# Kernel tuning notes

Hardware: AMD Instinct MI355X
Metric: run time of the kernel (lower is better)

Reference implementation:

```python
import jax, jax.numpy as jnp
import numpy as np

B, S, D, H = 2, 2048, 1024, 16
HD = D // H                      # 64
NUM_ROPE_DIMS = 2
NF = HD // (2 * NUM_ROPE_DIMS)   # 16 freqs per rope dim -> total HD//2
FFN_H = 4 * D


def householder_matrix(vs):
    """Product of Householder reflections: Q = prod_i (I - 2 v_i v_i^T / ||v_i||^2)."""
    dim = vs.shape[-1]
    def step(Q, v):
        v = v[:, None]
        Q = Q - (2.0 / (jnp.sum(v * v) + 1e-8)) * (v @ (v.T @ Q))
        return Q, None
    Q, _ = jax.lax.scan(step, jnp.eye(dim, dtype=vs.dtype), vs)
    return Q


def rmsnorm(x):
    # torch.nn.RMSNorm(eps=None) uses dtype eps, no affine
    return x * jax.lax.rsqrt(jnp.mean(x * x, axis=-1, keepdims=True) + jnp.finfo(x.dtype).eps)


def setup_inputs() -> dict:
    key = jax.random.key(0)
    ks = jax.random.split(key, 8)
    x = jax.random.normal(ks[0], (B, S, D), jnp.float32)
    mask = jnp.tril(jnp.ones((S, S), dtype=bool))          # causal block mask
    qkv_w = jax.random.normal(ks[1], (3 * D, D), jnp.float32) * 0.02
    out_w = jax.random.normal(ks[2], (D, D), jnp.float32) * 0.02
    gate_w = jax.random.normal(ks[3], (D, D), jnp.float32) * 0.02
    gate_b = jnp.zeros((D,), jnp.float32)
    w12 = jax.random.normal(ks[4], (2 * FFN_H, D), jnp.float32) * 0.02
    w3 = jax.random.normal(ks[5], (D, FFN_H), jnp.float32) * 0.02
    hh_vs = jax.random.normal(ks[6], (HD // 2, HD), jnp.float32) * 0.02
    inv_freq = 1.0 / (10000.0 ** (jnp.arange(NF, dtype=jnp.float32) / NF))
    pos = jnp.arange(S, dtype=jnp.float32)
    rope_pos = jnp.stack([pos, pos], axis=-1)              # [S, num_rope_dims]
    return dict(x=x, mask=mask, qkv_w=qkv_w, out_w=out_w, gate_w=gate_w,
                gate_b=gate_b, w12=w12, w3=w3, hh_vs=hh_vs,
                inv_freq=inv_freq, rope_pos=rope_pos)


def reference(x, mask, qkv_w, out_w, gate_w, gate_b, w12, w3, hh_vs, inv_freq, rope_pos):
    Bs, Ss, Ds = x.shape
    resid = x
    xn = rmsnorm(x)
    qkv = xn @ qkv_w.T                                      # [B,S,3D]
    q, k, v = jnp.split(qkv, 3, axis=-1)
    q = q.reshape(Bs, Ss, H, HD).transpose(0, 2, 1, 3)      # [B,H,S,HD]
    k = k.reshape(Bs, Ss, H, HD).transpose(0, 2, 1, 3)
    v = v.reshape(Bs, Ss, H, HD).transpose(0, 2, 1, 3)

    # RnRoPE: rotate into canonical basis, apply RoPE, rotate back
    Q = householder_matrix(hh_vs)                           # [HD,HD]
    q = q @ Q.T
    k = k @ Q.T
    # geo_state.scale = 1.0
    full = jnp.einsum('sd,f->sdf', rope_pos, inv_freq).reshape(Ss, -1)  # [S, HD//2]
    half = HD // 2
    full = full[:, :half]
    emb = jnp.concatenate([full, full], axis=-1)            # [S, HD]
    cos, sin = jnp.cos(emb), jnp.sin(emb)

    def rot(t):
        t1, t2 = jnp.split(t, 2, axis=-1)
        return t * cos + jnp.concatenate([-t2, t1], axis=-1) * sin

    q = rot(q) @ Q
    k = rot(k) @ Q

    # block-masked attention (flex_attention default scale = 1/sqrt(HD))
    scores = jnp.einsum('bhsd,bhtd->bhst', q, k) / jnp.sqrt(jnp.asarray(HD, x.dtype))
    scores = jnp.where(mask, scores, -jnp.inf)
    attn = jax.nn.softmax(scores, axis=-1)
    o = jnp.einsum('bhst,bhtd->bhsd', attn, v)
    o = o.transpose(0, 2, 1, 3).reshape(Bs, Ss, Ds)
    o = o @ out_w.T
    gate = jax.nn.sigmoid(o @ gate_w.T + gate_b)
    x = resid + o * gate

    # SwiGLU FFN
    resid2 = x
    xn2 = rmsnorm(x)
    x12 = xn2 @ w12.T
    x1, x2 = jnp.split(x12, 2, axis=-1)
    ffn = (jax.nn.silu(x1) * x2) @ w3.T
    return resid2 + ffn
```

## Files before the change

kernel.cpp:

```cpp
#include <hip/hip_runtime.h>
#include <hip/hip_bf16.h>
#include <math.h>

constexpr int Bc = 2, Sc = 2048, Dc = 1024, Hc = 16, HDc = 64;
constexpr int D3 = 3 * Dc;

typedef __bf16 bf16x8 __attribute__((ext_vector_type(8)));
typedef float f32x4 __attribute__((ext_vector_type(4)));

__device__ __forceinline__ void gll16(const void* g, void* l) {
  __builtin_amdgcn_global_load_lds((const __attribute__((address_space(1))) unsigned int*)g,
                                   (__attribute__((address_space(3))) unsigned int*)l,
                                   16, 0, 0);
}

__device__ __forceinline__ unsigned short f2bf(float v) {
  __hip_bfloat16 h = __float2bfloat16(v);
  return *(unsigned short*)&h;
}
__device__ __forceinline__ float b2f(unsigned short u) {
  unsigned v = ((unsigned)u) << 16;
  return __uint_as_float(v);
}

#define SBAR() asm volatile("s_barrier" ::: "memory")

__global__ __launch_bounds__(256) void f2b_kernel(const float* __restrict__ in,
                                                  unsigned short* __restrict__ out) {
  int i = blockIdx.x * 256 + threadIdx.x;
  float4 v = ((const float4*)in)[i];
  ushort4 o;
  o.x = f2bf(v.x); o.y = f2bf(v.y); o.z = f2bf(v.z); o.w = f2bf(v.w);
  ((ushort4*)out)[i] = o;
}

__global__ __launch_bounds__(256) void w12i_kernel(const float* __restrict__ in,
                                                   unsigned short* __restrict__ out) {
  int r = blockIdx.x;
  int g = r >> 5, u = r & 31;
  int src = ((u < 16) ? 0 : 4096) + g * 16 + (u & 15);
  float4 v = ((const float4*)(in + (size_t)src * 1024))[threadIdx.x];
  ushort4 o;
  o.x = f2bf(v.x); o.y = f2bf(v.y); o.z = f2bf(v.z); o.w = f2bf(v.w);
  ((ushort4*)(out + (size_t)r * 1024))[threadIdx.x] = o;
}

__global__ __launch_bounds__(256) void rmsnorm_bf16_kernel(const float* __restrict__ in,
                                                           unsigned short* __restrict__ out) {
  int row = blockIdx.x;
  const float4* x4 = (const float4*)(in + (size_t)row * Dc);
  float4 v = x4[threadIdx.x];
  float s = v.x * v.x + v.y * v.y + v.z * v.z + v.w * v.w;
#pragma unroll
  for (int off = 1; off < 64; off <<= 1) s += __shfl_xor(s, off);
  __shared__ float wsum[4];
  if ((threadIdx.x & 63) == 0) wsum[threadIdx.x >> 6] = s;
  __syncthreads();
  float tot = wsum[0] + wsum[1] + wsum[2] + wsum[3];
  float r = rsqrtf(tot * (1.0f / Dc) + 1.1920928955078125e-07f);
  ushort4 o;
  o.x = f2bf(v.x * r); o.y = f2bf(v.y * r); o.z = f2bf(v.z * r); o.w = f2bf(v.w * r);
  ((ushort4*)(out + (size_t)row * Dc))[threadIdx.x] = o;
}

__global__ __launch_bounds__(64) void hh_kernel(const float* __restrict__ vs,
                                                float* __restrict__ Qout) {
  __shared__ float Qm[64][65];
  __shared__ float vsh[64];
  int t = threadIdx.x;
  for (int i = 0; i < 64; ++i) Qm[i][t] = (i == t) ? 1.0f : 0.0f;
  for (int it = 0; it < 32; ++it) {
    __syncthreads();
    vsh[t] = vs[it * 64 + t];
    __syncthreads();
    float nv = 0.0f;
    for (int i = 0; i < 64; ++i) nv += vsh[i] * vsh[i];
    float c = 2.0f / (nv + 1e-8f);
    float wj = 0.0f;
    for (int i = 0; i < 64; ++i) wj += vsh[i] * Qm[i][t];
    for (int i = 0; i < 64; ++i) Qm[i][t] -= c * vsh[i] * wj;
  }
  __syncthreads();
  for (int i = 0; i < 64; ++i) Qout[i * 64 + t] = Qm[i][t];
}

__global__ __launch_bounds__(256) void wqk_kernel(const float* __restrict__ W,
                                                  const float* __restrict__ Qm,
                                                  unsigned short* __restrict__ out) {
  int n = blockIdx.x;
  int r = n & 63;
  int base = n & ~63;
  int t = threadIdx.x;
  float a0 = 0, a1 = 0, a2 = 0, a3 = 0;
  const float4* Wp = (const float4*)(W + (size_t)base * 1024) + t;
#pragma unroll 8
  for (int e = 0; e < 64; ++e) {
    float q = Qm[r * 64 + e];
    float4 wv = Wp[(size_t)e * 256];
    a0 += q * wv.x; a1 += q * wv.y; a2 += q * wv.z; a3 += q * wv.w;
  }
  float sc = (n < 1024) ? 0.18033688f : 1.0f;
  ushort4 o;
  o.x = f2bf(a0 * sc); o.y = f2bf(a1 * sc); o.z = f2bf(a2 * sc); o.w = f2bf(a3 * sc);
  ((ushort4*)(out + (size_t)n * 1024))[t] = o;
}

__global__ __launch_bounds__(256) void rtab_kernel(const float* __restrict__ rope_pos,
                                                   const float* __restrict__ inv_freq,
                                                   float2* __restrict__ tab) {
  int id = blockIdx.x * 256 + threadIdx.x;
  int s = id >> 5, d = id & 31;
  float pos = rope_pos[s * 2 + (d >> 4)];
  float emb = pos * inv_freq[d & 15];
  tab[id] = make_float2(cosf(emb), sinf(emb));
}

__global__ __launch_bounds__(256) void rope_kernel(const unsigned short* __restrict__ qkv,
                                                   const float2* __restrict__ tab,
                                                   unsigned short* __restrict__ qb,
                                                   unsigned short* __restrict__ kb) {
  int t = threadIdx.x;
  int gid = blockIdx.x * 64 + (t >> 2);
  int sub = t & 3;
  int h = gid & 15;
  int which = (gid >> 4) & 1;
  int tok = gid >> 5;
  int s = tok & (Sc - 1), b = tok >> 11;
  const unsigned short* src = qkv + (size_t)tok * D3 + which * Dc + h * 64 + sub * 8;
  uint4 lov = *(const uint4*)src;
  uint4 hiv = *(const uint4*)(src + 32);
  const unsigned short* lp = (const unsigned short*)&lov;
  const unsigned short* hp = (const unsigned short*)&hiv;
  unsigned short olo[8], ohi[8];
  const float2* tp = tab + s * 32 + sub * 8;
#pragma unroll
  for (int i = 0; i < 8; ++i) {
    float2 cs = tp[i];
    float lo = b2f(lp[i]), hi = b2f(hp[i]);
    olo[i] = f2bf(lo * cs.x - hi * cs.y);
    ohi[i] = f2bf(hi * cs.x + lo * cs.y);
  }
  unsigned short* dst = (which ? kb : qb) + ((size_t)((b * Hc + h) * Sc + s)) * 64 + sub * 8;
  *(uint4*)dst = *(uint4*)olo;
  *(uint4*)(dst + 32) = *(uint4*)ohi;
}

__global__ __launch_bounds__(256) void vt_kernel(const unsigned short* __restrict__ qkv,
                                                 unsigned short* __restrict__ vtb) {
  __shared__ unsigned short tile[64 * 72];
  int st = blockIdx.x;
  int bh = blockIdx.y;
  int b = bh >> 4, h = bh & 15;
  int t = threadIdx.x;
  int srow = t >> 2, c16 = (t & 3) * 16;
  const unsigned short* src =
      qkv + (size_t)(b * Sc + st * 64 + srow) * D3 + 2 * Dc + h * 64 + c16;
  uint4 a0 = *(const uint4*)src;
  uint4 a1 = *(const uint4*)(src + 8);
  *(uint4*)(tile + srow * 72 + c16) = a0;
  *(uint4*)(tile + srow * 72 + c16 + 8) = a1;
  __syncthreads();
  int d = t >> 2, sch = (t & 3) * 16;
  unsigned short tmp[16];
#pragma unroll
  for (int i = 0; i < 16; ++i) tmp[i] = tile[(sch + i) * 72 + d];
  unsigned short* dst = vtb + ((size_t)(bh * 64 + d)) * Sc + st * 64 + sch;
  *(uint4*)dst = *(uint4*)tmp;
  *(uint4*)(dst + 8) = *(uint4*)(tmp + 8);
}

template <int MODE>
__global__ __launch_bounds__(512, 1) void mgemm8p(const unsigned short* __restrict__ A,
                                                  const unsigned short* __restrict__ B,
                                                  unsigned short* __restrict__ C,
                                                  int M, int N, int K) {
  __shared__ unsigned short lds[65536];
  const int t = threadIdx.x;
  const int lane = t & 63;
  const int wave = t >> 6;
  const int wr = wave >> 2, wc = wave & 3;
  const int l15 = lane & 15, l4 = lane >> 4;
  const int gx = gridDim.x;
  const int nwg = gx * gridDim.y;
  const int id = blockIdx.y * gx + blockIdx.x;
  const int swz = (id & 7) * (nwg >> 3) + (id >> 3);
  const int m0 = (swz / gx) * 256;
  const int n0 = (swz % gx) * 256;
  const int NT = K >> 6;
  const int sko = (((t & 3) ^ ((t >> 3) & 3)) * 8);
  const unsigned short* ag0 = A + (size_t)(m0 + (t >> 2)) * K + sko;
  const unsigned short* ag1 = ag0 + (size_t)128 * K;
  const unsigned short* bg0 = B + (size_t)(n0 + (t >> 2)) * K + sko;
  const unsigned short* bg1 = bg0 + (size_t)128 * K;
  const int t8 = t * 8;
  const int ks = (l4 ^ ((l15 >> 1) & 3)) * 8;
  gll16(ag0, lds + t8);
  gll16(ag1, lds + 4096 + t8);
  gll16(bg0, lds + 32768 + t8);
  gll16(bg1, lds + 32768 + 4096 + t8);
  gll16(ag0 + 32, lds + 8192 + t8);
  gll16(ag1 + 32, lds + 8192 + 4096 + t8);
  gll16(bg0 + 32, lds + 32768 + 8192 + t8);
  gll16(bg1 + 32, lds + 32768 + 8192 + 4096 + t8);
  asm volatile("s_waitcnt vmcnt(4)" ::: "memory");
  SBAR();
  f32x4 acc[8][4] = {};
  for (int kt = 0; kt < NT; ++kt) {
    const int cur = (kt & 1) << 14;
    const int nxt = cur ^ 16384;
    const int kof = ((kt + 1 < NT) ? (kt + 1) : kt) << 6;
    const unsigned short* Ap = lds + cur;
    const unsigned short* Bp = lds + 32768 + cur;
    bf16x8 a[8], b0, b1;
#pragma unroll
    for (int i = 0; i < 8; ++i)
      a[i] = *(const bf16x8*)(Ap + (wr * 128 + i * 16 + l15) * 32 + ks);
    b0 = *(const bf16x8*)(Bp + (wc * 64 + l15) * 32 + ks);
    b1 = *(const bf16x8*)(Bp + (wc * 64 + 16 + l15) * 32 + ks);
    gll16(ag0 + kof, lds + nxt + t8);
    gll16(ag1 + kof, lds + nxt + 4096 + t8);
    SBAR();
    __builtin_amdgcn_s_setprio(1);
#pragma unroll
    for (int i = 0; i < 8; ++i) {
      acc[i][0] = __builtin_amdgcn_mfma_f32_16x16x32_bf16(a[i], b0, acc[i][0], 0, 0, 0);
      acc[i][1] = __builtin_amdgcn_mfma_f32_16x16x32_bf16(a[i], b1, acc[i][1], 0, 0, 0);
    }
    __builtin_amdgcn_s_setprio(0);
    SBAR();
    b0 = *(const bf16x8*)(Bp + (wc * 64 + 32 + l15) * 32 + ks);
    b1 = *(const bf16x8*)(Bp + (wc * 64 + 48 + l15) * 32 + ks);
    gll16(bg0 + kof, lds + 32768 + nxt + t8);
    gll16(bg1 + kof, lds + 32768 + nxt + 4096 + t8);
    asm volatile("s_waitcnt vmcnt(4)" ::: "memory");
    SBAR();
    __builtin_amdgcn_s_setprio(1);
#pragma unroll
    for (int i = 0; i < 8; ++i) {
      acc[i][2] = __builtin_amdgcn_mfma_f32_16x16x32_bf16(a[i], b0, acc[i][2], 0, 0, 0);
      acc[i][3] = __builtin_amdgcn_mfma_f32_16x16x32_bf16(a[i], b1, acc[i][3], 0, 0, 0);
    }
    __builtin_amdgcn_s_setprio(0);
    SBAR();
#pragma unroll
    for (int i = 0; i < 8; ++i)
      a[i] = *(const bf16x8*)(Ap + 8192 + (wr * 128 + i * 16 + l15) * 32 + ks);
    b0 = *(const bf16x8*)(Bp + 8192 + (wc * 64 + l15) * 32 + ks);
    b1 = *(const bf16x8*)(Bp + 8192 + (wc * 64 + 16 + l15) * 32 + ks);
    gll16(ag0 + kof + 32, lds + nxt + 8192 + t8);
    gll16(ag1 + kof + 32, lds + nxt + 8192 + 4096 + t8);
    SBAR();
    __builtin_amdgcn_s_setprio(1);
#pragma unroll
    for (int i = 0; i < 8; ++i) {
      acc[i][0] = __builtin_amdgcn_mfma_f32_16x16x32_bf16(a[i], b0, acc[i][0], 0, 0, 0);
      acc[i][1] = __builtin_amdgcn_mfma_f32_16x16x32_bf16(a[i], b1, acc[i][1], 0, 0, 0);
    }
    __builtin_amdgcn_s_setprio(0);
    SBAR();
    b0 = *(const bf16x8*)(Bp + 8192 + (wc * 64 + 32 + l15) * 32 + ks);
    b1 = *(const bf16x8*)(Bp + 8192 + (wc * 64 + 48 + l15) * 32 + ks);
    gll16(bg0 + kof + 32, lds + 32768 + nxt + 8192 + t8);
    gll16(bg1 + kof + 32, lds + 32768 + nxt + 8192 + 4096 + t8);
    asm volatile("s_waitcnt vmcnt(4)" ::: "memory");
    SBAR();
    __builtin_amdgcn_s_setprio(1);
#pragma unroll
    for (int i = 0; i < 8; ++i) {
      acc[i][2] = __builtin_amdgcn_mfma_f32_16x16x32_bf16(a[i], b0, acc[i][2], 0, 0, 0);
      acc[i][3] = __builtin_amdgcn_mfma_f32_16x16x32_bf16(a[i], b1, acc[i][3], 0, 0, 0);
    }
    __builtin_amdgcn_s_setprio(0);
    SBAR();
  }
  asm volatile("s_waitcnt vmcnt(0)" ::: "memory");
  const int r0 = m0 + wr * 128 + l4 * 4;
  if (MODE == 0) {
    const int c0 = n0 + wc * 64 + l15;
#pragma unroll
    for (int i = 0; i < 8; ++i)
#pragma unroll
      for (int j = 0; j < 4; ++j)
#pragma unroll
        for (int r = 0; r < 4; ++r)
          C[(size_t)(r0 + i * 16 + r) * N + c0 + j * 16] = f2bf(acc[i][j][r]);
  } else {
    const int nc = N >> 1;
    const int c0 = (n0 >> 1) + wc * 32 + l15;
#pragma unroll
    for (int i = 0; i < 8; ++i)
#pragma unroll
      for (int p = 0; p < 2; ++p)
#pragma unroll
        for (int r = 0; r < 4; ++r) {
          float v = acc[i][2 * p][r];
          float sv = v / (1.0f + __expf(-v));
          C[(size_t)(r0 + i * 16 + r) * nc + c0 + p * 16] = f2bf(sv * acc[i][2 * p + 1][r]);
        }
  }
}

template <int MODE>
__global__ __launch_bounds__(256, 3) void mgemm64(const unsigned short* __restrict__ A,
                                                  const unsigned short* __restrict__ W,
                                                  const float* __restrict__ R,
                                                  const float* __restrict__ R2,
                                                  const float* __restrict__ bias,
                                                  void* __restrict__ Cout,
                                                  void* __restrict__ Cout2,
                                                  int M, int N, int K) {
  __shared__ unsigned short As[2][2048];
  __shared__ unsigned short Bs[2][4096];
  const int t = threadIdx.x;
  const int lane = t & 63;
  const int wave = t >> 6;
  const int wr = wave >> 1, wc = wave & 1;
  const int m0 = blockIdx.y * 64, n0 = blockIdx.x * 128;
  f32x4 acc[2][4] = {};
  const int srow = t >> 2;
  const int sch = (((t & 3) ^ ((t >> 3) & 3)) * 8);
  const unsigned short* Ag = A + (size_t)(m0 + srow) * K + sch;
  const unsigned short* Wg = W + (size_t)(n0 + srow) * K + sch;
  const size_t rstep = (size_t)64 * K;
  const int frow = lane & 15;
  const int l4 = lane >> 4;
  const int fk = (l4 ^ ((frow >> 1) & 3)) * 8;
  gll16(Ag, As[0] + t * 8);
  gll16(Wg, Bs[0] + t * 8);
  gll16(Wg + rstep, Bs[0] + 2048 + t * 8);
  for (int k0 = 0; k0 < K; k0 += 32) {
    const int cur = (k0 >> 5) & 1;
    const int kn = (k0 + 32 < K) ? (k0 + 32) : k0;
    gll16(Ag + kn, As[cur ^ 1] + t * 8);
    gll16(Wg + kn, Bs[cur ^ 1] + t * 8);
    gll16(Wg + kn + rstep, Bs[cur ^ 1] + 2048 + t * 8);
    asm volatile("s_waitcnt vmcnt(3)" ::: "memory");
    SBAR();
    bf16x8 af[2], bq[4];
#pragma unroll
    for (int i = 0; i < 2; ++i)
      af[i] = *(const bf16x8*)(As[cur] + (wr * 32 + i * 16 + frow) * 32 + fk);
#pragma unroll
    for (int j = 0; j < 4; ++j)
      bq[j] = *(const bf16x8*)(Bs[cur] + (wc * 64 + j * 16 + frow) * 32 + fk);
    __builtin_amdgcn_s_setprio(1);
#pragma unroll
    for (int i = 0; i < 2; ++i)
#pragma unroll
      for (int j = 0; j < 4; ++j)
        acc[i][j] = __builtin_amdgcn_mfma_f32_16x16x32_bf16(af[i], bq[j], acc[i][j], 0, 0, 0);
    __builtin_amdgcn_s_setprio(0);
    SBAR();
  }
  asm volatile("s_waitcnt vmcnt(0)" ::: "memory");
  const int crow = wr * 32 + (lane >> 4) * 4;
  const int ccol = wc * 64 + (lane & 15);
#pragma unroll
  for (int i = 0; i < 2; ++i) {
#pragma unroll
    for (int j = 0; j < 4; ++j) {
#pragma unroll
      for (int r = 0; r < 4; ++r) {
        int row = m0 + crow + i * 16 + r;
        int col = n0 + ccol + j * 16;
        float v = acc[i][j][r];
        size_t off = (size_t)row * N + col;
        if (MODE == 2) {
          ((float*)Cout)[off] = v + R[off];
        } else if (MODE == 4) {
          ((float*)Cout)[off] = v;
          ((unsigned short*)Cout2)[off] = f2bf(v);
        } else {
          float g = v + bias[col];
          float sg = 1.0f / (1.0f + __expf(-g));
          ((float*)Cout)[off] = R[off] + R2[off] * sg;
        }
      }
    }
  }
}

__global__ __launch_bounds__(256, 3) void mattn(const unsigned short* __restrict__ qb,
                                                const unsigned short* __restrict__ kb,
                                                const unsigned short* __restrict__ vtb,
                                                unsigned short* __restrict__ out) {
  __shared__ unsigned short Qs[8192];
  __shared__ unsigned short Ks[2][4096];
  __shared__ unsigned short Vts[4096];
  __shared__ unsigned short Ps[4 * 16 * 72];
  const int qt = gridDim.x - 1 - blockIdx.x;
  const int bh = blockIdx.y;
  const int b = bh >> 4, h = bh & 15;
  const int t = threadIdx.x, lane = t & 63, w = t >> 6;
  const int l15 = lane & 15, l4 = lane >> 4;
  const unsigned short* qbase = qb + ((size_t)bh * Sc + qt * 128) * 64;
  const unsigned short* kbase = kb + (size_t)bh * Sc * 64;
  const unsigned short* vbase = vtb + (size_t)bh * 64 * Sc;
#pragma unroll
  for (int i = 0; i < 4; ++i) {
    int idx = t + i * 256;
    int r = idx >> 3;
    int cg = (idx & 7) ^ (r & 7);
    gll16(qbase + (size_t)r * 64 + cg * 8, Qs + idx * 8);
  }
  const int sr = t >> 3;
  const int scg = (t & 7) ^ (sr & 7);
  gll16(vbase + (size_t)sr * Sc + scg * 8, Vts + t * 8);
  gll16(vbase + (size_t)(sr + 32) * Sc + scg * 8, Vts + 2048 + t * 8);
  gll16(kbase + (size_t)sr * 64 + scg * 8, Ks[0] + t * 8);
  gll16(kbase + (size_t)(sr + 32) * 64 + scg * 8, Ks[0] + 2048 + t * 8);
  bf16x8 qf[2][2];
  f32x4 oacc[2][4] = {};
  float lrow[2][4] = {};
  unsigned short* pw = Ps + w * 16 * 72;
  const int ktmax = 2 * qt + 1;
  for (int kt = 0; kt <= ktmax; ++kt) {
    const int cur = kt & 1;
    if (kt > 0) {
      gll16(vbase + (size_t)sr * Sc + kt * 64 + scg * 8, Vts + t * 8);
      gll16(vbase + (size_t)(sr + 32) * Sc + kt * 64 + scg * 8, Vts + 2048 + t * 8);
    }
    const int ktn = (kt < ktmax) ? kt + 1 : kt;
    gll16(kbase + (size_t)(ktn * 64 + sr) * 64 + scg * 8, Ks[cur ^ 1] + t * 8);
    gll16(kbase + (size_t)(ktn * 64 + sr + 32) * 64 + scg * 8, Ks[cur ^ 1] + 2048 + t * 8);
    if (kt == 0) {
      asm volatile("s_waitcnt vmcnt(2)" ::: "memory");
    } else {
      asm volatile("s_waitcnt vmcnt(4)" ::: "memory");
    }
    SBAR();
    if (kt == 0) {
#pragma unroll
      for (int ch = 0; ch < 2; ++ch) {
        int qrow = ch * 64 + w * 16 + l15;
#pragma unroll
        for (int kc = 0; kc < 2; ++kc)
          qf[ch][kc] = *(const bf16x8*)(Qs + qrow * 64 + (((kc * 4 + l4) ^ (l15 & 7)) * 8));
      }
    }
    const bool actA = (kt <= 2 * qt);
    f32x4 sc[2][4] = {};
#pragma unroll
    for (int kc = 0; kc < 2; ++kc) {
      bf16x8 kf[4];
#pragma unroll
      for (int j = 0; j < 4; ++j)
        kf[j] = *(const bf16x8*)(Ks[cur] + (j * 16 + l15) * 64 + (((kc * 4 + l4) ^ (l15 & 7)) * 8));
      __builtin_amdgcn_s_setprio(1);
      if (actA) {
#pragma unroll
        for (int j = 0; j < 4; ++j)
          sc[0][j] = __builtin_amdgcn_mfma_f32_16x16x32_bf16(qf[0][kc], kf[j], sc[0][j], 0, 0, 0);
      }
#pragma unroll
      for (int j = 0; j < 4; ++j)
        sc[1][j] = __builtin_amdgcn_mfma_f32_16x16x32_bf16(qf[1][kc], kf[j], sc[1][j], 0, 0, 0);
      __builtin_amdgcn_s_setprio(0);
    }
    const int rl = w * 16 + l4 * 4;
    if (kt == 2 * qt) {
#pragma unroll
      for (int j = 0; j < 4; ++j)
#pragma unroll
        for (int r = 0; r < 4; ++r)
          if (j * 16 + l15 > rl + r) sc[0][j][r] = -INFINITY;
    }
    if (kt == ktmax) {
#pragma unroll
      for (int j = 0; j < 4; ++j)
#pragma unroll
        for (int r = 0; r < 4; ++r)
          if (j * 16 + l15 > rl + r) sc[1][j][r] = -INFINITY;
    }
    asm volatile("s_waitcnt vmcnt(2)" ::: "memory");
    SBAR();
    bf16x8 vf[2][4];
#pragma unroll
    for (int kc = 0; kc < 2; ++kc)
#pragma unroll
      for (int j = 0; j < 4; ++j)
        vf[kc][j] = *(const bf16x8*)(Vts + (j * 16 + l15) * 64 + (((kc * 4 + l4) ^ (l15 & 7)) * 8));
#pragma unroll
    for (int ch = 0; ch < 2; ++ch) {
      if (ch == 0 && !actA) continue;
#pragma unroll
      for (int j = 0; j < 4; ++j)
#pragma unroll
        for (int r = 0; r < 4; ++r) {
          float p = exp2f(sc[ch][j][r]);
          lrow[ch][r] += p;
          pw[(l4 * 4 + r) * 72 + j * 16 + l15] = f2bf(p);
        }
      __asm__ __volatile__("s_waitcnt lgkmcnt(0)" ::: "memory");
      __builtin_amdgcn_s_setprio(1);
#pragma unroll
      for (int kc = 0; kc < 2; ++kc) {
        bf16x8 pf = *(const bf16x8*)(pw + l15 * 72 + kc * 32 + l4 * 8);
#pragma unroll
        for (int j = 0; j < 4; ++j)
          oacc[ch][j] = __builtin_amdgcn_mfma_f32_16x16x32_bf16(pf, vf[kc][j], oacc[ch][j], 0, 0, 0);
      }
      __builtin_amdgcn_s_setprio(0);
    }
    SBAR();
  }
  asm volatile("s_waitcnt vmcnt(0)" ::: "memory");
#pragma unroll
  for (int ch = 0; ch < 2; ++ch) {
#pragma unroll
    for (int r = 0; r < 4; ++r) {
      float s = lrow[ch][r];
      s += __shfl_xor(s, 1);
      s += __shfl_xor(s, 2);
      s += __shfl_xor(s, 4);
      s += __shfl_xor(s, 8);
      float inv = 1.0f / s;
#pragma unroll
      for (int j = 0; j < 4; ++j) {
        int srow = qt * 128 + ch * 64 + w * 16 + l4 * 4 + r;
        out[((size_t)(b * Sc + srow)) * Dc + h * 64 + j * 16 + l15] =
            f2bf(oacc[ch][j][r] * inv);
      }
    }
  }
}

extern "C" void kernel_launch(void* const* d_in, const int* in_sizes, int n_in,
                              void* d_out, int out_size, void* d_ws, size_t ws_size,
                              hipStream_t stream) {
  const float* x        = (const float*)d_in[0];
  const float* qkv_w    = (const float*)d_in[2];
  const float* out_w    = (const float*)d_in[3];
  const float* gate_w   = (const float*)d_in[4];
  const float* gate_b   = (const float*)d_in[5];
  const float* w12      = (const float*)d_in[6];
  const float* w3       = (const float*)d_in[7];
  const float* hh_vs    = (const float*)d_in[8];
  const float* inv_freq = (const float*)d_in[9];
  const float* rope_pos = (const float*)d_in[10];
  char* ws = (char*)d_ws;
  unsigned short* woutb  = (unsigned short*)(ws + 0);
  float2*         rtab   = (float2*)(ws + 2097152);
  unsigned short* wqkvb  = (unsigned short*)(ws + 4194304);
  unsigned short* attnb  = (unsigned short*)(ws + 4194304);
  float*          xmid   = (float*)(ws + 0);
  unsigned short* slotB  = (unsigned short*)(ws + 16777216);
  float*          oproj  = (float*)(ws + 25165824);
  unsigned short* w12b   = (unsigned short*)(ws + 25165824);
  unsigned short* wgateb = (unsigned short*)(ws + 41943040);
  unsigned short* w3b    = (unsigned short*)(ws + 41943040);
  unsigned short* qkvb   = (unsigned short*)(ws + 58720256);
  unsigned short* hbufb  = (unsigned short*)(ws + 58720256);
  unsigned short* qb     = (unsigned short*)(ws + 83886080);
  unsigned short* oprojb = (unsigned short*)(ws + 83886080);
  unsigned short* kb     = (unsigned short*)(ws + 92274688);
  unsigned short* vtb    = (unsigned short*)(ws + 100663296);
  float*          Qb     = (float*)(ws + 109051904);
  float* outp = (float*)d_out;

  hh_kernel<<<1, 64, 0, stream>>>(hh_vs, Qb);
  rtab_kernel<<<256, 256, 0, stream>>>(rope_pos, inv_freq, rtab);
  wqk_kernel<<<2048, 256, 0, stream>>>(qkv_w, Qb, wqkvb);
  f2b_kernel<<<1024, 256, 0, stream>>>(qkv_w + 2048 * 1024,
                                       wqkvb + 2048 * 1024);
  f2b_kernel<<<1024, 256, 0, stream>>>(out_w, woutb);
  f2b_kernel<<<1024, 256, 0, stream>>>(gate_w, wgateb);
  rmsnorm_bf16_kernel<<<4096, 256, 0, stream>>>(x, slotB);
  mgemm8p<0><<<dim3(12, 16), 512, 0, stream>>>(slotB, wqkvb, qkvb, 4096, 3072, 1024);
  rope_kernel<<<2048, 256, 0, stream>>>(qkvb, rtab, qb, kb);
  vt_kernel<<<dim3(32, 32), 256, 0, stream>>>(qkvb, vtb);
  mattn<<<dim3(16, 32), 256, 0, stream>>>(qb, kb, vtb, attnb);
  mgemm64<4><<<dim3(8, 64), 256, 0, stream>>>(attnb, woutb, nullptr, nullptr, nullptr,
                                              oproj, oprojb, 4096, 1024, 1024);
  mgemm64<5><<<dim3(8, 64), 256, 0, stream>>>(oprojb, wgateb, x, oproj, gate_b,
                                              xmid, nullptr, 4096, 1024, 1024);
  w12i_kernel<<<8192, 256, 0, stream>>>(w12, w12b);
  f2b_kernel<<<4096, 256, 0, stream>>>(w3, w3b);
  rmsnorm_bf16_kernel<<<4096, 256, 0, stream>>>(xmid, slotB);
  mgemm8p<1><<<dim3(32, 16), 512, 0, stream>>>(slotB, w12b, hbufb, 4096, 8192, 1024);
  mgemm64<2><<<dim3(8, 64), 256, 0, stream>>>(hbufb, w3b, xmid, nullptr, nullptr,
                                              outp, nullptr, 4096, 1024, 4096);
}
```

Measured before the change: 539.9 us.

## Split causal attention KV range across blocks and combine partials

The attention kernel now splits each query tile's causal KV range into chunks of at most 8 KV tiles, launching 40 blocks per head instead of 16 to balance the triangular workload. Each block writes unnormalized fp32 partial outputs and row sums, and a new combine kernel sums the partials and normalizes to bf16. This works without max-rescaling because the original kernel already skipped the running max. The gate weight conversion is moved later and its buffer relocated to avoid overlapping the new partial buffers. The extra partial-buffer traffic and an extra launch trade against better load balance and occupancy.

```diff
diff --git a/kernel.cpp b/kernel.cpp
--- a/kernel.cpp
+++ b/kernel.cpp
@@ -383,14 +383,22 @@
 __global__ __launch_bounds__(256, 3) void mattn(const unsigned short* __restrict__ qb,
                                                 const unsigned short* __restrict__ kb,
                                                 const unsigned short* __restrict__ vtb,
-                                                unsigned short* __restrict__ out) {
+                                                float* __restrict__ opart,
+                                                float* __restrict__ lpart) {
   __shared__ unsigned short Qs[8192];
   __shared__ unsigned short Ks[2][4096];
   __shared__ unsigned short Vts[4096];
   __shared__ unsigned short Ps[4 * 16 * 72];
-  const int qt = gridDim.x - 1 - blockIdx.x;
+  const int bidx = 39 - blockIdx.x;
+  int qt, s;
+  if (bidx < 4)       { qt = bidx;                  s = 0; }
+  else if (bidx < 12) { qt = 4 + ((bidx - 4) >> 1); s = (bidx - 4) & 1; }
+  else if (bidx < 24) { int u = bidx - 12; int q3 = u / 3; qt = 8 + q3; s = u - 3 * q3; }
+  else                { qt = 12 + ((bidx - 24) >> 2); s = (bidx - 24) & 3; }
+  const int nt = 2 * qt + 2;
+  const int kt0 = s * 8;
+  const int kt1 = (kt0 + 8 < nt) ? kt0 + 8 : nt;
   const int bh = blockIdx.y;
-  const int b = bh >> 4, h = bh & 15;
   const int t = threadIdx.x, lane = t & 63, w = t >> 6;
   const int l15 = lane & 15, l4 = lane >> 4;
   const unsigned short* qbase = qb + ((size_t)bh * Sc + qt * 128) * 64;
@@ -405,31 +413,30 @@
   }
   const int sr = t >> 3;
   const int scg = (t & 7) ^ (sr & 7);
-  gll16(vbase + (size_t)sr * Sc + scg * 8, Vts + t * 8);
-  gll16(vbase + (size_t)(sr + 32) * Sc + scg * 8, Vts + 2048 + t * 8);
-  gll16(kbase + (size_t)sr * 64 + scg * 8, Ks[0] + t * 8);
-  gll16(kbase + (size_t)(sr + 32) * 64 + scg * 8, Ks[0] + 2048 + t * 8);
+  gll16(vbase + (size_t)sr * Sc + kt0 * 64 + scg * 8, Vts + t * 8);
+  gll16(vbase + (size_t)(sr + 32) * Sc + kt0 * 64 + scg * 8, Vts + 2048 + t * 8);
+  gll16(kbase + (size_t)(kt0 * 64 + sr) * 64 + scg * 8, Ks[0] + t * 8);
+  gll16(kbase + (size_t)(kt0 * 64 + sr + 32) * 64 + scg * 8, Ks[0] + 2048 + t * 8);
   bf16x8 qf[2][2];
   f32x4 oacc[2][4] = {};
   float lrow[2][4] = {};
   unsigned short* pw = Ps + w * 16 * 72;
-  const int ktmax = 2 * qt + 1;
-  for (int kt = 0; kt <= ktmax; ++kt) {
+  for (int kt = kt0; kt < kt1; ++kt) {
     const int cur = kt & 1;
-    if (kt > 0) {
+    if (kt > kt0) {
       gll16(vbase + (size_t)sr * Sc + kt * 64 + scg * 8, Vts + t * 8);
       gll16(vbase + (size_t)(sr + 32) * Sc + kt * 64 + scg * 8, Vts + 2048 + t * 8);
     }
-    const int ktn = (kt < ktmax) ? kt + 1 : kt;
+    const int ktn = (kt + 1 < kt1) ? kt + 1 : kt;
     gll16(kbase + (size_t)(ktn * 64 + sr) * 64 + scg * 8, Ks[cur ^ 1] + t * 8);
     gll16(kbase + (size_t)(ktn * 64 + sr + 32) * 64 + scg * 8, Ks[cur ^ 1] + 2048 + t * 8);
-    if (kt == 0) {
+    if (kt == kt0) {
       asm volatile("s_waitcnt vmcnt(2)" ::: "memory");
     } else {
       asm volatile("s_waitcnt vmcnt(4)" ::: "memory");
     }
     SBAR();
-    if (kt == 0) {
+    if (kt == kt0) {
 #pragma unroll
       for (int ch = 0; ch < 2; ++ch) {
         int qrow = ch * 64 + w * 16 + l15;
@@ -465,7 +472,7 @@
         for (int r = 0; r < 4; ++r)
           if (j * 16 + l15 > rl + r) sc[0][j][r] = -INFINITY;
     }
-    if (kt == ktmax) {
+    if (kt == 2 * qt + 1) {
 #pragma unroll
       for (int j = 0; j < 4; ++j)
 #pragma unroll
@@ -505,23 +512,59 @@
     SBAR();
   }
   asm volatile("s_waitcnt vmcnt(0)" ::: "memory");
+  float* opr = opart + ((size_t)(bh * 40 + bidx) * 128) * 64;
+  float* lpr = lpart + (bh * 40 + bidx) * 128;
 #pragma unroll
   for (int ch = 0; ch < 2; ++ch) {
 #pragma unroll
     for (int r = 0; r < 4; ++r) {
-      float s = lrow[ch][r];
-      s += __shfl_xor(s, 1);
-      s += __shfl_xor(s, 2);
-      s += __shfl_xor(s, 4);
-      s += __shfl_xor(s, 8);
-      float inv = 1.0f / s;
-#pragma unroll
-      for (int j = 0; j < 4; ++j) {
-        int srow = qt * 128 + ch * 64 + w * 16 + l4 * 4 + r;
-        out[((size_t)(b * Sc + srow)) * Dc + h * 64 + j * 16 + l15] =
-            f2bf(oacc[ch][j][r] * inv);
-      }
-    }
+      float sum = lrow[ch][r];
+      sum += __shfl_xor(sum, 1);
+      sum += __shfl_xor(sum, 2);
+      sum += __shfl_xor(sum, 4);
+      sum += __shfl_xor(sum, 8);
+      const int row = ch * 64 + w * 16 + l4 * 4 + r;
+      if (l15 == 0) lpr[row] = sum;
+#pragma unroll
+      for (int j = 0; j < 4; ++j)
+        opr[(size_t)row * 64 + j * 16 + l15] = oacc[ch][j][r];
+    }
+  }
+}
+
+__global__ __launch_bounds__(256) void acomb(const float* __restrict__ Op,
+                                             const float* __restrict__ lp,
+                                             unsigned short* __restrict__ out) {
+  const int qt = blockIdx.x, bh = blockIdx.y;
+  const int b = bh >> 4, h = bh & 15;
+  const int ns = (qt >> 2) + 1;
+  const int base = (qt < 4) ? qt
+                 : (qt < 8) ? 4 + 2 * (qt - 4)
+                 : (qt < 12) ? 12 + 3 * (qt - 8)
+                 : 24 + 4 * (qt - 12);
+  const int t = threadIdx.x;
+  const int row = t >> 1, d0 = (t & 1) * 32;
+  float l = 0.0f;
+  float acc[32] = {};
+  for (int s = 0; s < ns; ++s) {
+    const int pidx = bh * 40 + base + s;
+    l += lp[pidx * 128 + row];
+    const float4* src = (const float4*)(Op + ((size_t)pidx * 128 + row) * 64 + d0);
+#pragma unroll
+    for (int i = 0; i < 8; ++i) {
+      float4 v = src[i];
+      acc[i * 4 + 0] += v.x; acc[i * 4 + 1] += v.y;
+      acc[i * 4 + 2] += v.z; acc[i * 4 + 3] += v.w;
+    }
+  }
+  const float inv = 1.0f / l;
+  unsigned short* dst = out + ((size_t)(b * Sc + qt * 128 + row)) * Dc + h * 64 + d0;
+#pragma unroll
+  for (int i = 0; i < 8; ++i) {
+    ushort4 o;
+    o.x = f2bf(acc[i * 4 + 0] * inv); o.y = f2bf(acc[i * 4 + 1] * inv);
+    o.z = f2bf(acc[i * 4 + 2] * inv); o.w = f2bf(acc[i * 4 + 3] * inv);
+    ((ushort4*)dst)[i] = o;
   }
 }
 
@@ -543,13 +586,15 @@
   float2*         rtab   = (float2*)(ws + 2097152);
   unsigned short* wqkvb  = (unsigned short*)(ws + 4194304);
   unsigned short* attnb  = (unsigned short*)(ws + 4194304);
+  float*          lpart  = (float*)(ws + 12582912);
   float*          xmid   = (float*)(ws + 0);
   unsigned short* slotB  = (unsigned short*)(ws + 16777216);
+  float*          opart  = (float*)(ws + 16777216);
   float*          oproj  = (float*)(ws + 25165824);
   unsigned short* w12b   = (unsigned short*)(ws + 25165824);
-  unsigned short* wgateb = (unsigned short*)(ws + 41943040);
   unsigned short* w3b    = (unsigned short*)(ws + 41943040);
   unsigned short* qkvb   = (unsigned short*)(ws + 58720256);
+  unsigned short* wgateb = (unsigned short*)(ws + 58720256);
   unsigned short* hbufb  = (unsigned short*)(ws + 58720256);
   unsigned short* qb     = (unsigned short*)(ws + 83886080);
   unsigned short* oprojb = (unsigned short*)(ws + 83886080);
@@ -564,12 +609,13 @@
   f2b_kernel<<<1024, 256, 0, stream>>>(qkv_w + 2048 * 1024,
                                        wqkvb + 2048 * 1024);
   f2b_kernel<<<1024, 256, 0, stream>>>(out_w, woutb);
-  f2b_kernel<<<1024, 256, 0, stream>>>(gate_w, wgateb);
   rmsnorm_bf16_kernel<<<4096, 256, 0, stream>>>(x, slotB);
   mgemm8p<0><<<dim3(12, 16), 512, 0, stream>>>(slotB, wqkvb, qkvb, 4096, 3072, 1024);
   rope_kernel<<<2048, 256, 0, stream>>>(qkvb, rtab, qb, kb);
   vt_kernel<<<dim3(32, 32), 256, 0, stream>>>(qkvb, vtb);
-  mattn<<<dim3(16, 32), 256, 0, stream>>>(qb, kb, vtb, attnb);
+  f2b_kernel<<<1024, 256, 0, stream>>>(gate_w, wgateb);
+  mattn<<<dim3(40, 32), 256, 0, stream>>>(qb, kb, vtb, opart, lpart);
+  acomb<<<dim3(16, 32), 256, 0, stream>>>(opart, lpart, attnb);
   mgemm64<4><<<dim3(8, 64), 256, 0, stream>>>(attnb, woutb, nullptr, nullptr, nullptr,
                                               oproj, oprojb, 4096, 1024, 1024);
   mgemm64<5><<<dim3(8, 64), 256, 0, stream>>>(oprojb, wgateb, x, oproj, gate_b,
```

Result: no change. 538.6 us (-0.2%).
